# Kernel tuning notes

Hardware: AMD Instinct MI355X
Metric: run time of the kernel (lower is better)

Reference implementation:

```python
import jax, jax.numpy as jnp
import numpy as np

EPS = 1e-5

def _bilinear_sample(xb, ys, xs):
    # xb: [C,H,W]; ys, xs: [H,W] float sample coordinates (zero outside bounds)
    C, H, W = xb.shape
    y0 = jnp.floor(ys); x0 = jnp.floor(xs)
    y1 = y0 + 1.0;      x1 = x0 + 1.0
    wy1 = ys - y0; wy0 = 1.0 - wy1
    wx1 = xs - x0; wx0 = 1.0 - wx1
    def g(yi, xi):
        valid = (yi >= 0) & (yi < H) & (xi >= 0) & (xi < W)
        yc = jnp.clip(yi, 0, H - 1).astype(jnp.int32)
        xc = jnp.clip(xi, 0, W - 1).astype(jnp.int32)
        return xb[:, yc, xc] * valid[None].astype(xb.dtype)  # [C,H,W]
    return (g(y0, x0) * (wy0 * wx0)[None] + g(y0, x1) * (wy0 * wx1)[None]
          + g(y1, x0) * (wy1 * wx0)[None] + g(y1, x1) * (wy1 * wx1)[None])

def _deform_conv2d(x, offset, mask, w, b):
    # x:[B,C,H,W] offset:[B,18,H,W] mask:[B,9,H,W] w:[Co,C,3,3] b:[Co]
    B, C, H, W = x.shape
    Co = w.shape[0]
    ii = jnp.arange(H, dtype=x.dtype)[:, None]
    jj = jnp.arange(W, dtype=x.dtype)[None, :]
    cols = []
    for k in range(9):  # fixed 3x3 kernel positions, row-major (dy=offset[2k], dx=offset[2k+1])
        ky, kx = k // 3 - 1, k % 3 - 1
        ys = ii + ky + offset[:, 2 * k]      # [B,H,W]
        xs = jj + kx + offset[:, 2 * k + 1]
        v = jax.vmap(_bilinear_sample)(x, ys, xs)  # [B,C,H,W]
        cols.append(v * mask[:, k][:, None])
    cols = jnp.stack(cols, axis=1)               # [B,9,C,H,W]
    out = jnp.einsum('bkchw,ock->bohw', cols, w.reshape(Co, C, 9))
    return out + b[None, :, None, None]

def setup_inputs() -> dict:
    key = jax.random.key(0)
    k1, k2, k3, k4 = jax.random.split(key, 4)
    B, Cin, Cout, H, W = 8, 64, 64, 128, 128
    x = jax.random.normal(k1, (B, Cin, H, W), dtype=jnp.float32)
    # offset/mask conv: small weights so learned offsets stay O(1) pixels;
    # bias[18:]=2.0 as in the module's init (masks start near sigmoid(2))
    w_off = jax.random.normal(k2, (27, Cin, 3, 3), dtype=jnp.float32) * 0.01
    b_off = jnp.concatenate([jnp.zeros((18,), jnp.float32), jnp.full((9,), 2.0, jnp.float32)])
    w_dcn = jax.random.normal(k3, (Cout, Cin, 3, 3), dtype=jnp.float32) / np.sqrt(Cin * 9)
    b_dcn = jax.random.normal(k4, (Cout,), dtype=jnp.float32) * 0.01
    return {"x": x, "w_off": w_off, "b_off": b_off, "w_dcn": w_dcn, "b_dcn": b_dcn}

def reference(x, w_off, b_off, w_dcn, b_dcn):
    dn = ('NCHW', 'OIHW', 'NCHW')
    om = jax.lax.conv_general_dilated(x, w_off, (1, 1), 'SAME', dimension_numbers=dn)
    om = om + b_off[None, :, None, None]
    offset = om[:, :18]
    mask = jax.nn.sigmoid(om[:, 18:])
    y = _deform_conv2d(x, offset, mask, w_dcn, b_dcn)
    # InstanceNorm2d (affine=False, biased variance) + ReLU
    mu = jnp.mean(y, axis=(2, 3), keepdims=True)
    var = jnp.var(y, axis=(2, 3), keepdims=True)
    y = (y - mu) * jax.lax.rsqrt(var + EPS)
    return jax.nn.relu(y)
```

## Files before the change

kernel.cpp:

```cpp
#include <hip/hip_runtime.h>
#include <hip/hip_fp16.h>

#define BB   8
#define CIN  64
#define COUT 64
#define HH   128
#define WW   128
#define HWSZ (HH * WW)

typedef _Float16 f16x8 __attribute__((ext_vector_type(8)));
typedef _Float16 h2v   __attribute__((ext_vector_type(2)));
typedef float    f32x4 __attribute__((ext_vector_type(4)));

__device__ __forceinline__ unsigned short f2h_u(float f) {
    __half h = __float2half(f);
    return __half_as_ushort(h);
}
__device__ __forceinline__ float h2f_u(unsigned short u) {
    _Float16 f = *(_Float16*)&u;
    return (float)f;
}
__device__ __forceinline__ unsigned pk2h(float lo, float hi) {
    return (unsigned)f2h_u(lo) | ((unsigned)f2h_u(hi) << 16);
}
__device__ __forceinline__ h2v dupL(unsigned u) { h2v v = *(h2v*)&u; return (h2v){v[0], v[0]}; }
__device__ __forceinline__ h2v dupH(unsigned u) { h2v v = *(h2v*)&u; return (h2v){v[1], v[1]}; }

__device__ __forceinline__ unsigned comb2h(unsigned a, unsigned b, unsigned c, unsigned d,
                                           h2v W0, h2v W1, h2v W2, h2v W3) {
    h2v A = *(h2v*)&a, B = *(h2v*)&b, C = *(h2v*)&c, D = *(h2v*)&d;
    h2v r = A * W0;
    r += B * W1;
    r += C * W2;
    r += D * W3;
    return *(unsigned*)&r;
}


__global__ __launch_bounds__(256) void k_tr(const float* __restrict__ x,
                                            const float* __restrict__ wd,
                                            const float* __restrict__ wof,
                                            unsigned short* __restrict__ xT,
                                            unsigned short* __restrict__ wdT,
                                            unsigned short* __restrict__ wofT,
                                            float4* __restrict__ sums4)
{
    const int t = threadIdx.x;
    const int id = blockIdx.x;
    if (id >= 512) {
        if (id == 512) sums4[t] = make_float4(0.f, 0.f, 0.f, 0.f);
        int base = (id - 512) * 256 + t;
#pragma unroll
        for (int j = 0; j < 4; ++j) {
            int idx = base + j * 16384;
            if (idx < 36864) {
                int k = idx >> 12, rem = idx & 4095, co = rem >> 6, c = rem & 63;
                wdT[idx] = f2h_u(wd[(co * 64 + c) * 9 + k]);
            } else if (idx < 55296) {
                int jj = idx - 36864;
                int k = jj >> 11, rem = jj & 2047, o = rem >> 6, c = rem & 63;
                wofT[jj] = (o < 27) ? f2h_u(wof[(o * 64 + c) * 9 + k]) : 0;
            }
        }
        return;
    }
    __shared__ unsigned short tile[256 * 66];
    const int b = id & 7;
    const int p0 = (id >> 3) * 256;
#pragma unroll
    for (int i = 0; i < 16; ++i) {
        int c = i * 4 + (t >> 6);
        int pl = (t & 63) * 4;
        float4 v = *(const float4*)(x + (((size_t)b * 64 + c) << 14) + p0 + pl);
        tile[(pl + 0) * 66 + c] = f2h_u(v.x);
        tile[(pl + 1) * 66 + c] = f2h_u(v.y);
        tile[(pl + 2) * 66 + c] = f2h_u(v.z);
        tile[(pl + 3) * 66 + c] = f2h_u(v.w);
    }
    __syncthreads();
#pragma unroll
    for (int i = 0; i < 8; ++i) {
        int idd = i * 256 + t;
        int pt = idd >> 3, ck = idd & 7;
        const unsigned* srcp = (const unsigned*)&tile[pt * 66 + ck * 8];
        uint4 r;
        r.x = srcp[0]; r.y = srcp[1]; r.z = srcp[2]; r.w = srcp[3];
        *(uint4*)(xT + ((size_t)b << 20) + ((size_t)(ck >> 2) << 19)
                     + (size_t)(p0 + pt) * 32 + (ck & 3) * 8) = r;
    }
}

__global__ __launch_bounds__(512) void k_fused(
    const unsigned short* __restrict__ xT, const unsigned short* __restrict__ wdT,
    const unsigned short* __restrict__ wofT, const float* __restrict__ bof,
    const float* __restrict__ bd, unsigned short* __restrict__ yh,
    float2* __restrict__ sums)
{
    __shared__ unsigned short tile_sh[8 * 128 * 32];
    __shared__ unsigned short om_sh[27 * 512];
    __shared__ uint4          meta_sh[8][64];

    const int t = threadIdx.x;
    const int lane = t & 63, wv = t >> 6;
    const int q = lane >> 4, l15 = lane & 15;
    const int b = blockIdx.x & 7;
    const int pblk = (blockIdx.x >> 3) * 512;
    const int p = pblk + t;
    const int h = p >> 7, w = p & 127;
    const int h0 = pblk >> 7;
    const unsigned short* xbS = xT + ((size_t)b << 20);
    const int gch = q * 8;

    const int hrow = h0 + (wv >> 1);
    const int c0 = (wv & 1) * 64;

#define STAGE(HF) { \
    const unsigned short* xs_ = xbS + ((HF) << 19); \
    _Pragma("unroll") \
    for (int i_ = 0; i_ < 8; ++i_) { \
        int idx_ = i_ * 512 + t; \
        int s_ = idx_ >> 9, u_ = idx_ & 511; \
        int y_ = h0 - 2 + s_; \
        y_ = min(max(y_, 0), HH - 1); \
        uint4 v_ = *(const uint4*)(xs_ + (size_t)y_ * (WW * 32) + u_ * 8); \
        *(uint4*)&tile_sh[idx_ * 8] = v_; \
    } }

    f32x4 aoff[2][4];
#pragma unroll
    for (int mt = 0; mt < 2; ++mt)
#pragma unroll
        for (int nt = 0; nt < 4; ++nt) aoff[mt][nt] = (f32x4){0.f, 0.f, 0.f, 0.f};

    for (int hf = 0; hf < 2; ++hf) {
        __syncthreads();
        STAGE(hf);
        __syncthreads();
#pragma unroll
        for (int k = 0; k < 9; ++k) {
            const int ky = k / 3 - 1, kx = k % 3 - 1;
            if ((unsigned)(hrow + ky) < (unsigned)HH) {
                const int trow = hrow + ky - (h0 - 2);
                const unsigned short* wk = wofT + k * 2048;
                f16x8 af[2];
#pragma unroll
                for (int mt = 0; mt < 2; ++mt)
                    af[mt] = *(const f16x8*)(wk + (mt * 16 + l15) * 64 + hf * 32 + q * 8);
                f16x8 bfr[4];
#pragma unroll
                for (int nt = 0; nt < 4; ++nt) {
                    int tc = c0 + nt * 16 + l15 + kx;
                    int tcc = min(max(tc, 0), WW - 1);
                    f16x8 bv = *(const f16x8*)&tile_sh[trow * 4096 + tcc * 32 + q * 8];
                    if ((unsigned)tc >= (unsigned)WW)
                        bv = (f16x8){(_Float16)0, (_Float16)0, (_Float16)0, (_Float16)0,
                                     (_Float16)0, (_Float16)0, (_Float16)0, (_Float16)0};
                    bfr[nt] = bv;
                }
#pragma unroll
                for (int mt = 0; mt < 2; ++mt)
#pragma unroll
                    for (int nt = 0; nt < 4; ++nt)
                        aoff[mt][nt] = __builtin_amdgcn_mfma_f32_16x16x32_f16(
                            af[mt], bfr[nt], aoff[mt][nt], 0, 0, 0);
            }
        }
    }
    {
        const int pw = (wv >> 1) * 128 + c0;
#pragma unroll
        for (int mt = 0; mt < 2; ++mt)
#pragma unroll
            for (int r = 0; r < 4; ++r) {
                int o = mt * 16 + q * 4 + r;
                if (o < 27) {
                    float bias = bof[o];
#pragma unroll
                    for (int nt = 0; nt < 4; ++nt) {
                        float v = aoff[mt][nt][r] + bias;
                        if (o >= 18) v = 1.f / (1.f + __expf(-v));
                        om_sh[o * 512 + pw + nt * 16 + l15] = f2h_u(v);
                    }
                }
            }
    }
    __syncthreads();

    f32x4 acc[4][4];
#pragma unroll
    for (int mt = 0; mt < 4; ++mt)
#pragma unroll
        for (int g = 0; g < 4; ++g) acc[mt][g] = (f32x4){0.f, 0.f, 0.f, 0.f};

#define LOADG2(P, g) { \
    unsigned d0_ = M[g].x; \
    unsigned b0_ = (d0_ & 0x000fffffu) + gch; \
    unsigned sx_ = (d0_ >> 19) & 32u;       \
    unsigned sy_ = (d0_ >> 13) & 4096u;     \
    unsigned b1_ = b0_ + sx_; \
    if (__builtin_expect((int)(d0_ >> 31), 0)) { \
        P[0] = *(const uint4*)(xbh + b0_); \
        P[1] = *(const uint4*)(xbh + b1_); \
        P[2] = *(const uint4*)(xbh + b0_ + sy_); \
        P[3] = *(const uint4*)(xbh + b1_ + sy_); \
    } else { \
        P[0] = *(const uint4*)&tile_sh[b0_]; \
        P[1] = *(const uint4*)&tile_sh[b1_]; \
        P[2] = *(const uint4*)&tile_sh[b0_ + sy_]; \
        P[3] = *(const uint4*)&tile_sh[b1_ + sy_]; \
    } }

#define COMB2(DST, P, g) { \
    h2v W0_ = dupL(M[g].y), W2_ = dupH(M[g].y); \
    h2v W1_ = dupL(M[g].z), W3_ = dupH(M[g].z); \
    uint4 R_; \
    R_.x = comb2h(P[0].x, P[1].x, P[2].x, P[3].x, W0_, W1_, W2_, W3_); \
    R_.y = comb2h(P[0].y, P[1].y, P[2].y, P[3].y, W0_, W1_, W2_, W3_); \
    R_.z = comb2h(P[0].z, P[1].z, P[2].z, P[3].z, W0_, W1_, W2_, W3_); \
    R_.w = comb2h(P[0].w, P[1].w, P[2].w, P[3].w, W0_, W1_, W2_, W3_); \
    DST = *(f16x8*)&R_; }

    for (int pass = 0; pass < 2; ++pass) {
        const int hfg = 1 - pass;
        if (pass == 1) {
            __syncthreads();
            STAGE(0);
            __syncthreads();
        }
        const unsigned short* xbh = xbS + (hfg << 19);

        float offy = h2f_u(om_sh[0 * 512 + t]);
        float offx = h2f_u(om_sh[1 * 512 + t]);
        float mk   = h2f_u(om_sh[18 * 512 + t]);

        for (int k = 0; k < 9; ++k) {
            float ys = (float)(h + (k / 3) - 1) + offy;
            float xs = (float)(w + (k % 3) - 1) + offx;
            float fy0 = floorf(ys), fx0 = floorf(xs);
            float wy1 = ys - fy0, wx1 = xs - fx0;
            float wy0 = 1.f - wy1, wx0 = 1.f - wx1;
            int y0 = (int)fy0, x0 = (int)fx0;
            int y1 = y0 + 1, x1 = x0 + 1;
            bool vy0 = (y0 >= 0) && (y0 < HH), vy1 = (y1 >= 0) && (y1 < HH);
            bool vx0 = (x0 >= 0) && (x0 < WW), vx1 = (x1 >= 0) && (x1 < WW);
            int y0c = min(max(y0, 0), HH - 1), y1c = min(max(y1, 0), HH - 1);
            int x0c = min(max(x0, 0), WW - 1), x1c = min(max(x1, 0), WW - 1);
            bool ft = (y0c < h0 - 2) || (y1c > h0 + 5);
            unsigned d0;
            if (!ft) d0 = (unsigned)((y0c - h0 + 2) * 4096 + x0c * 32);
            else     d0 = 0x80000000u | (unsigned)((y0c * WW + x0c) * 32);
            if (x1c != x0c) d0 |= 0x01000000u;
            if (y1c != y0c) d0 |= 0x02000000u;
            float w00 = (vy0 && vx0) ? mk * wy0 * wx0 : 0.f;
            float w01 = (vy0 && vx1) ? mk * wy0 * wx1 : 0.f;
            float w10 = (vy1 && vx0) ? mk * wy1 * wx0 : 0.f;
            float w11 = (vy1 && vx1) ? mk * wy1 * wx1 : 0.f;
            meta_sh[wv][lane] = make_uint4(d0, pk2h(w00, w10), pk2h(w01, w11), 0u);
            int kn = (k < 8) ? k + 1 : 8;
            offy = h2f_u(om_sh[(2 * kn) * 512 + t]);
            offx = h2f_u(om_sh[(2 * kn + 1) * 512 + t]);
            mk   = h2f_u(om_sh[(18 + kn) * 512 + t]);
            __builtin_amdgcn_wave_barrier();

            uint4 M[4];
#pragma unroll
            for (int g = 0; g < 4; ++g)
                M[g] = meta_sh[wv][g * 16 + l15];

            const unsigned short* wk = wdT + k * 4096;
            f16x8 af_[4];
#pragma unroll
            for (int mt = 0; mt < 4; ++mt)
                af_[mt] = *(const f16x8*)(wk + (mt * 16 + l15) * 64 + (hfg << 5) + q * 8);

            f16x8 bfr[4];
            uint4 pb[3][4];
            LOADG2(pb[0], 0);
            LOADG2(pb[1], 1);
#pragma unroll
            for (int g = 0; g < 4; ++g) {
                if (g + 2 < 4) LOADG2(pb[(g + 2) % 3], g + 2);
                COMB2(bfr[g], pb[g % 3], g);
            }

#pragma unroll
            for (int mt = 0; mt < 4; ++mt)
#pragma unroll
                for (int g = 0; g < 4; ++g)
                    acc[mt][g] = __builtin_amdgcn_mfma_f32_16x16x32_f16(
                        af_[mt], bfr[g], acc[mt][g], 0, 0, 0);
        }
    }
#undef LOADG2
#undef COMB2
#undef STAGE

    __syncthreads();
    float* redS = (float*)&meta_sh[0][0];
    float* redQ = redS + 512;
    const int p0 = pblk + wv * 64;
    unsigned short* yb = yh + (size_t)b * COUT * HWSZ;
#pragma unroll
    for (int mt = 0; mt < 4; ++mt)
#pragma unroll
        for (int r = 0; r < 4; ++r) {
            int co = mt * 16 + q * 4 + r;
            float bias = bd[co];
            float s = 0.f, qq = 0.f;
#pragma unroll
            for (int g = 0; g < 4; ++g) {
                float v = acc[mt][g][r] + bias;
                yb[(size_t)co * HWSZ + p0 + g * 16 + l15] = f2h_u(v);
                s += v; qq += v * v;
            }
#pragma unroll
            for (int m = 1; m < 16; m <<= 1) {
                s += __shfl_xor(s, m);
                qq += __shfl_xor(qq, m);
            }
            if (l15 == 0) { redS[wv * 64 + co] = s; redQ[wv * 64 + co] = qq; }
        }
    __syncthreads();
    if (t < 64) {
        float S = 0.f, Q = 0.f;
#pragma unroll
        for (int wvi = 0; wvi < 8; ++wvi) {
            S += redS[wvi * 64 + t];
            Q += redQ[wvi * 64 + t];
        }
        atomicAdd(&sums[b * 64 + t].x, S);
        atomicAdd(&sums[b * 64 + t].y, Q);
    }
}

__global__ __launch_bounds__(256) void k_norm(const unsigned short* __restrict__ yh,
                                              float* __restrict__ out,
                                              const float2* __restrict__ sums)
{
    const int id = blockIdx.x;
    const int b = id & 7;
    const int rest = id >> 3;
    const int co = rest >> 3;
    const int off = rest & 7;
    const int bco = b * 64 + co;
    float2 sq = sums[bco];
    float mu  = sq.x * (1.f / (float)HWSZ);
    float var = sq.y * (1.f / (float)HWSZ) - mu * mu;
    float rstd = rsqrtf(var + 1e-5f);
    const int base = (bco << 14) + off * 2048 + threadIdx.x * 8;
    uint4 v8 = *(const uint4*)(yh + base);
    float4 o0, o1;
    o0.x = fmaxf((h2f_u((unsigned short)(v8.x & 0xffffu)) - mu) * rstd, 0.f);
    o0.y = fmaxf((h2f_u((unsigned short)(v8.x >> 16))     - mu) * rstd, 0.f);
    o0.z = fmaxf((h2f_u((unsigned short)(v8.y & 0xffffu)) - mu) * rstd, 0.f);
    o0.w = fmaxf((h2f_u((unsigned short)(v8.y >> 16))     - mu) * rstd, 0.f);
    o1.x = fmaxf((h2f_u((unsigned short)(v8.z & 0xffffu)) - mu) * rstd, 0.f);
    o1.y = fmaxf((h2f_u((unsigned short)(v8.z >> 16))     - mu) * rstd, 0.f);
    o1.z = fmaxf((h2f_u((unsigned short)(v8.w & 0xffffu)) - mu) * rstd, 0.f);
    o1.w = fmaxf((h2f_u((unsigned short)(v8.w >> 16))     - mu) * rstd, 0.f);
    *(float4*)(out + base)     = o0;
    *(float4*)(out + base + 4) = o1;
}

extern "C" void kernel_launch(void* const* d_in, const int* in_sizes, int n_in,
                              void* d_out, int out_size, void* d_ws, size_t ws_size,
                              hipStream_t stream) {
    const float* x   = (const float*)d_in[0];
    const float* wof = (const float*)d_in[1];
    const float* bof = (const float*)d_in[2];
    const float* wd  = (const float*)d_in[3];
    const float* bd  = (const float*)d_in[4];
    float* out = (float*)d_out;

    char* ws = (char*)d_ws;
    unsigned short* xT   = (unsigned short*)ws;
    unsigned short* yh   = (unsigned short*)(ws + 16777216);
    unsigned short* wdT  = (unsigned short*)(ws + 33554432);
    unsigned short* wofT = (unsigned short*)(ws + 33628160);
    float2*         sums = (float2*)(ws + 33665024);

    k_tr    <<<576, 256, 0, stream>>>(x, wd, wof, xT, wdT, wofT, (float4*)sums);
    k_fused <<<256, 512, 0, stream>>>(xT, wdT, wofT, bof, bd, yh, sums);
    k_norm  <<<4096, 256, 0, stream>>>(yh, out, (const float2*)sums);
}
```

Baseline: 144.4 us.

## Drop fp16 NHWC pre-transpose; stage fp32 NCHW input directly in fused kernel

Removes the separate transpose/convert pass that wrote an fp16 channel-last copy of x. The fused kernel now reads fp32 NCHW x directly, converting and transposing into shared memory during staging. Far-sample fallbacks gather eight strided fp32 values per channel group from global memory. This saves one full read and write of the input tensor and a launch, but staging reads are strided across channels and fallback gathers become much less coalesced.

```diff
diff --git a/kernel.cpp b/kernel.cpp
--- a/kernel.cpp
+++ b/kernel.cpp
@@ -36,62 +36,32 @@
     return *(unsigned*)&r;
 }
 
-
-__global__ __launch_bounds__(256) void k_tr(const float* __restrict__ x,
-                                            const float* __restrict__ wd,
+__global__ __launch_bounds__(256) void k_wt(const float* __restrict__ wd,
                                             const float* __restrict__ wof,
-                                            unsigned short* __restrict__ xT,
                                             unsigned short* __restrict__ wdT,
                                             unsigned short* __restrict__ wofT,
                                             float4* __restrict__ sums4)
 {
     const int t = threadIdx.x;
     const int id = blockIdx.x;
-    if (id >= 512) {
-        if (id == 512) sums4[t] = make_float4(0.f, 0.f, 0.f, 0.f);
-        int base = (id - 512) * 256 + t;
-#pragma unroll
-        for (int j = 0; j < 4; ++j) {
-            int idx = base + j * 16384;
-            if (idx < 36864) {
-                int k = idx >> 12, rem = idx & 4095, co = rem >> 6, c = rem & 63;
-                wdT[idx] = f2h_u(wd[(co * 64 + c) * 9 + k]);
-            } else if (idx < 55296) {
-                int jj = idx - 36864;
-                int k = jj >> 11, rem = jj & 2047, o = rem >> 6, c = rem & 63;
-                wofT[jj] = (o < 27) ? f2h_u(wof[(o * 64 + c) * 9 + k]) : 0;
-            }
-        }
-        return;
-    }
-    __shared__ unsigned short tile[256 * 66];
-    const int b = id & 7;
-    const int p0 = (id >> 3) * 256;
-#pragma unroll
-    for (int i = 0; i < 16; ++i) {
-        int c = i * 4 + (t >> 6);
-        int pl = (t & 63) * 4;
-        float4 v = *(const float4*)(x + (((size_t)b * 64 + c) << 14) + p0 + pl);
-        tile[(pl + 0) * 66 + c] = f2h_u(v.x);
-        tile[(pl + 1) * 66 + c] = f2h_u(v.y);
-        tile[(pl + 2) * 66 + c] = f2h_u(v.z);
-        tile[(pl + 3) * 66 + c] = f2h_u(v.w);
-    }
-    __syncthreads();
-#pragma unroll
-    for (int i = 0; i < 8; ++i) {
-        int idd = i * 256 + t;
-        int pt = idd >> 3, ck = idd & 7;
-        const unsigned* srcp = (const unsigned*)&tile[pt * 66 + ck * 8];
-        uint4 r;
-        r.x = srcp[0]; r.y = srcp[1]; r.z = srcp[2]; r.w = srcp[3];
-        *(uint4*)(xT + ((size_t)b << 20) + ((size_t)(ck >> 2) << 19)
-                     + (size_t)(p0 + pt) * 32 + (ck & 3) * 8) = r;
+    if (id == 0) sums4[t] = make_float4(0.f, 0.f, 0.f, 0.f);
+    int base = id * 256 + t;
+#pragma unroll
+    for (int j = 0; j < 4; ++j) {
+        int idx = base + j * 16384;
+        if (idx < 36864) {
+            int k = idx >> 12, rem = idx & 4095, co = rem >> 6, c = rem & 63;
+            wdT[idx] = f2h_u(wd[(co * 64 + c) * 9 + k]);
+        } else if (idx < 55296) {
+            int jj = idx - 36864;
+            int k = jj >> 11, rem = jj & 2047, o = rem >> 6, c = rem & 63;
+            wofT[jj] = (o < 27) ? f2h_u(wof[(o * 64 + c) * 9 + k]) : 0;
+        }
     }
 }
 
 __global__ __launch_bounds__(512) void k_fused(
-    const unsigned short* __restrict__ xT, const unsigned short* __restrict__ wdT,
+    const float* __restrict__ x, const unsigned short* __restrict__ wdT,
     const unsigned short* __restrict__ wofT, const float* __restrict__ bof,
     const float* __restrict__ bd, unsigned short* __restrict__ yh,
     float2* __restrict__ sums)
@@ -108,22 +78,29 @@
     const int p = pblk + t;
     const int h = p >> 7, w = p & 127;
     const int h0 = pblk >> 7;
-    const unsigned short* xbS = xT + ((size_t)b << 20);
+    const float* xF = x + (size_t)b * 64 * HWSZ;
     const int gch = q * 8;
 
     const int hrow = h0 + (wv >> 1);
     const int c0 = (wv & 1) * 64;
 
-#define STAGE(HF) { \
-    const unsigned short* xs_ = xbS + ((HF) << 19); \
+#define STAGE_X(HF) { \
+    const float* xp_ = xF + (size_t)((HF) * 32) * HWSZ; \
     _Pragma("unroll") \
     for (int i_ = 0; i_ < 8; ++i_) { \
-        int idx_ = i_ * 512 + t; \
-        int s_ = idx_ >> 9, u_ = idx_ & 511; \
-        int y_ = h0 - 2 + s_; \
-        y_ = min(max(y_, 0), HH - 1); \
-        uint4 v_ = *(const uint4*)(xs_ + (size_t)y_ * (WW * 32) + u_ * 8); \
-        *(uint4*)&tile_sh[idx_ * 8] = v_; \
+        int idx_ = i_ * 512 + t;             \
+        int s_  = idx_ >> 9;                 \
+        int c2_ = idx_ & 15;                 \
+        int g_  = (idx_ >> 4) & 31;          \
+        int y_ = min(max(h0 - 2 + s_, 0), HH - 1); \
+        const float* pa_ = xp_ + (size_t)(2 * c2_) * HWSZ + y_ * WW + g_ * 4; \
+        float4 v0_ = *(const float4*)pa_; \
+        float4 v1_ = *(const float4*)(pa_ + HWSZ); \
+        unsigned short* wp_ = &tile_sh[s_ * 4096 + g_ * 128 + 2 * c2_]; \
+        *(unsigned*)(wp_ +  0) = pk2h(v0_.x, v1_.x); \
+        *(unsigned*)(wp_ + 32) = pk2h(v0_.y, v1_.y); \
+        *(unsigned*)(wp_ + 64) = pk2h(v0_.z, v1_.z); \
+        *(unsigned*)(wp_ + 96) = pk2h(v0_.w, v1_.w); \
     } }
 
     f32x4 aoff[2][4];
@@ -134,7 +111,7 @@
 
     for (int hf = 0; hf < 2; ++hf) {
         __syncthreads();
-        STAGE(hf);
+        STAGE_X(hf);
         __syncthreads();
 #pragma unroll
         for (int k = 0; k < 9; ++k) {
@@ -192,18 +169,30 @@
 #pragma unroll
         for (int g = 0; g < 4; ++g) acc[mt][g] = (f32x4){0.f, 0.f, 0.f, 0.f};
 
+#define FBLOAD(DST, pix_) { \
+    const float* fp_ = xFq + (pix_); \
+    uint4 R_; \
+    R_.x = pk2h(fp_[0],        fp_[HWSZ]); \
+    R_.y = pk2h(fp_[2 * HWSZ], fp_[3 * HWSZ]); \
+    R_.z = pk2h(fp_[4 * HWSZ], fp_[5 * HWSZ]); \
+    R_.w = pk2h(fp_[6 * HWSZ], fp_[7 * HWSZ]); \
+    DST = R_; }
+
 #define LOADG2(P, g) { \
     unsigned d0_ = M[g].x; \
-    unsigned b0_ = (d0_ & 0x000fffffu) + gch; \
-    unsigned sx_ = (d0_ >> 19) & 32u;       \
-    unsigned sy_ = (d0_ >> 13) & 4096u;     \
-    unsigned b1_ = b0_ + sx_; \
     if (__builtin_expect((int)(d0_ >> 31), 0)) { \
-        P[0] = *(const uint4*)(xbh + b0_); \
-        P[1] = *(const uint4*)(xbh + b1_); \
-        P[2] = *(const uint4*)(xbh + b0_ + sy_); \
-        P[3] = *(const uint4*)(xbh + b1_ + sy_); \
+        unsigned pix_ = d0_ & 0x000fffffu; \
+        unsigned dx_  = (d0_ >> 24) & 1u; \
+        unsigned dy_  = ((d0_ >> 25) & 1u) * WW; \
+        FBLOAD(P[0], pix_); \
+        FBLOAD(P[1], pix_ + dx_); \
+        FBLOAD(P[2], pix_ + dy_); \
+        FBLOAD(P[3], pix_ + dy_ + dx_); \
     } else { \
+        unsigned b0_ = (d0_ & 0x000fffffu) + gch; \
+        unsigned sx_ = (d0_ >> 19) & 32u;       \
+        unsigned sy_ = (d0_ >> 13) & 4096u;     \
+        unsigned b1_ = b0_ + sx_; \
         P[0] = *(const uint4*)&tile_sh[b0_]; \
         P[1] = *(const uint4*)&tile_sh[b1_]; \
         P[2] = *(const uint4*)&tile_sh[b0_ + sy_]; \
@@ -224,10 +213,10 @@
         const int hfg = 1 - pass;
         if (pass == 1) {
             __syncthreads();
-            STAGE(0);
+            STAGE_X(0);
             __syncthreads();
         }
-        const unsigned short* xbh = xbS + (hfg << 19);
+        const float* xFq = xF + (size_t)(hfg * 32 + q * 8) * HWSZ;
 
         float offy = h2f_u(om_sh[0 * 512 + t]);
         float offx = h2f_u(om_sh[1 * 512 + t]);
@@ -248,7 +237,7 @@
             bool ft = (y0c < h0 - 2) || (y1c > h0 + 5);
             unsigned d0;
             if (!ft) d0 = (unsigned)((y0c - h0 + 2) * 4096 + x0c * 32);
-            else     d0 = 0x80000000u | (unsigned)((y0c * WW + x0c) * 32);
+            else     d0 = 0x80000000u | (unsigned)(y0c * WW + x0c);
             if (x1c != x0c) d0 |= 0x01000000u;
             if (y1c != y0c) d0 |= 0x02000000u;
             float w00 = (vy0 && vx0) ? mk * wy0 * wx0 : 0.f;
@@ -292,8 +281,9 @@
         }
     }
 #undef LOADG2
+#undef FBLOAD
 #undef COMB2
-#undef STAGE
+#undef STAGE_X
 
     __syncthreads();
     float* redS = (float*)&meta_sh[0][0];
@@ -373,13 +363,12 @@
     float* out = (float*)d_out;
 
     char* ws = (char*)d_ws;
-    unsigned short* xT   = (unsigned short*)ws;
-    unsigned short* yh   = (unsigned short*)(ws + 16777216);
-    unsigned short* wdT  = (unsigned short*)(ws + 33554432);
-    unsigned short* wofT = (unsigned short*)(ws + 33628160);
-    float2*         sums = (float2*)(ws + 33665024);
-
-    k_tr    <<<576, 256, 0, stream>>>(x, wd, wof, xT, wdT, wofT, (float4*)sums);
-    k_fused <<<256, 512, 0, stream>>>(xT, wdT, wofT, bof, bd, yh, sums);
+    unsigned short* yh   = (unsigned short*)ws;
+    unsigned short* wdT  = (unsigned short*)(ws + 16777216);
+    unsigned short* wofT = (unsigned short*)(ws + 16850944);
+    float2*         sums = (float2*)(ws + 16887808);
+
+    k_wt    <<<64, 256, 0, stream>>>(wd, wof, wdT, wofT, (float4*)sums);
+    k_fused <<<256, 512, 0, stream>>>(x, wdT, wofT, bof, bd, yh, sums);
     k_norm  <<<4096, 256, 0, stream>>>(yh, out, (const float2*)sums);
 }
```

New measurement: 168.0 us. 1.16x slower.
